# Kernel tuning notes

Measured on AMD Instinct MI355X. Metric: run time of the kernel, lower is better.

Reference implementation:

```python
import jax, jax.numpy as jnp
import numpy as np

B, S, D = 2, 2048, 1024
E, K = 8, 2
CAP_FACTOR = 1.25
HID = 4 * D


def _capacity(num_tokens: int) -> int:
    import math
    cap = math.floor(K * CAP_FACTOR * num_tokens / E)
    cap += cap % 2
    return max(int(cap), 2)


def setup_inputs() -> dict:
    key = jax.random.key(0)
    k1, k2, k3, k4 = jax.random.split(key, 4)
    x = jax.random.normal(k1, (B, S, D), dtype=jnp.float32)
    w_gate = jax.random.normal(k2, (D, E), dtype=jnp.float32) * 0.02
    w_fc = jax.random.normal(k3, (E, D, HID), dtype=jnp.float32) * 0.02
    w_proj = jax.random.normal(k4, (E, HID, D), dtype=jnp.float32) * 0.02
    return {"x": x, "w_gate": w_gate, "w_fc": w_fc, "w_proj": w_proj}


def _moe_forward(x, w_gate, w_fc, w_proj):
    b, s, d = x.shape
    T = b * s
    cap = _capacity(T)
    xf = x.astype(jnp.float32).reshape(T, d)

    # --- Router (fp32, eval mode: no noise) ---
    logits = xf @ w_gate                                   # [T, E]
    top_v, top_i = jax.lax.top_k(logits, K)                # [T, K]
    NEG = jnp.float32(-1e30)
    masked = jnp.full_like(logits, NEG)
    masked = masked.at[jnp.arange(T)[:, None], top_i].set(top_v)
    probs = jax.nn.softmax(masked, axis=-1)                # [T, E], zero off top-k

    # --- Capacity assignment: cumsum over (k-major, token) flattened order ---
    oh = jax.nn.one_hot(top_i, E, dtype=jnp.int32)         # [T, K, E]
    oh = jnp.transpose(oh, (1, 0, 2))                      # [K, T, E]
    rank = jnp.cumsum(oh.reshape(K * T, E), axis=0).reshape(K, T, E) - 1
    within = (oh > 0) & (rank < cap)                       # [K, T, E]
    rank_sel = jnp.sum(jnp.where(within, rank, 0), axis=-1)  # [K, T]
    kept = jnp.any(within, axis=-1)                        # [K, T]

    p = jnp.take_along_axis(probs, top_i, axis=-1).T       # [K, T]
    w = jnp.where(kept, p, 0.0)                            # combine weights

    e_idx = top_i.T                                        # [K, T]
    t_idx = jnp.broadcast_to(jnp.arange(T)[None, :], (K, T))

    # expert_weights[t, e, c] (sparse scatter == torch one-hot combine)
    expert_weights = jnp.zeros((T, E, cap), jnp.float32)
    expert_weights = expert_weights.at[t_idx.ravel(), e_idx.ravel(), rank_sel.ravel()].add(w.ravel())

    # dispatch: expert_batches[e, c, :] = x of token routed to (e, c)
    disp = jnp.where(kept, 1.0, 0.0).ravel()[:, None]      # [K*T, 1]
    expert_batches = jnp.zeros((E, cap, d), jnp.float32)
    expert_batches = expert_batches.at[e_idx.ravel(), rank_sel.ravel()].add(disp * xf[t_idx.ravel()])

    # --- Expert MLPs (batched GEMMs, exact GELU, no bias, eval dropout) ---
    h = jnp.einsum('ecd,edh->ech', expert_batches, w_fc)
    h = jax.nn.gelu(h, approximate=False)
    expert_out = jnp.einsum('ech,ehd->ecd', h, w_proj)      # [E, cap, d]

    # --- Combine: gather expert outputs back to tokens weighted by router prob ---
    gathered = expert_out[e_idx.ravel(), rank_sel.ravel()].reshape(K, T, d)
    out_flat = jnp.sum(w[:, :, None] * gathered, axis=0)    # [T, d]
    output = out_flat.reshape(b, s, d)

    # --- Load balance loss (Switch) ---
    probs_full = jax.nn.softmax(logits, axis=-1)
    prob_per_expert = jnp.mean(probs_full, axis=0)          # [E]
    tokens_per_expert = jax.lax.stop_gradient(
        jnp.sum((expert_weights > 0).astype(jnp.float32), axis=(0, 2)) / (T * K)
    )
    lb_loss = E * jnp.sum(prob_per_expert * tokens_per_expert)

    # --- Router z-loss ---
    z_loss = jnp.mean(jax.nn.logsumexp(logits, axis=-1) ** 2)
    return output, lb_loss, z_loss


def reference(x, w_gate, w_fc, w_proj):
    return _moe_forward(x, w_gate, w_fc, w_proj)
```

## Files before the change

kernel.cpp:

```cpp
#include <hip/hip_runtime.h>
#include <hip/hip_bf16.h>
#include <cstdint>
#include <cstddef>

#define T_TOK 4096
#define D_DIM 1024
#define E_EXP 8
#define KSEL 2
#define CAP 1280
#define HID_DIM 4096

typedef __attribute__((ext_vector_type(8))) __bf16 bf16x8;
typedef __attribute__((ext_vector_type(4))) float floatx4;

__device__ __forceinline__ unsigned short f2bf(float f) {
  unsigned int u = __builtin_bit_cast(unsigned int, f);
  u = (u + 0x7FFFu + ((u >> 16) & 1u)) >> 16;
  return (unsigned short)u;
}
__device__ __forceinline__ float bf2f(unsigned short h) {
  unsigned int u = ((unsigned int)h) << 16;
  return __builtin_bit_cast(float, u);
}

__global__ void router_kernel(const float* __restrict__ x, const float* __restrict__ wg,
                              int* __restrict__ top1, int* __restrict__ top2,
                              float* __restrict__ p0, float* __restrict__ p1,
                              float* __restrict__ probsum, float* __restrict__ zsum) {
  __shared__ float lps[E_EXP];
  __shared__ float lz;
  if (threadIdx.x < E_EXP) lps[threadIdx.x] = 0.f;
  if (threadIdx.x == 0) lz = 0.f;
  __syncthreads();
  int wave = threadIdx.x >> 6;
  int lane = threadIdx.x & 63;
  int t = blockIdx.x * 4 + wave;
  const float* xr = x + (size_t)t * D_DIM;
  float acc[E_EXP];
#pragma unroll
  for (int e = 0; e < E_EXP; ++e) acc[e] = 0.f;
  for (int j = 0; j < D_DIM / 64; ++j) {
    int i = lane + 64 * j;
    float xv = xr[i];
    const float4* wr = (const float4*)(wg + (size_t)i * E_EXP);
    float4 w0 = wr[0], w1 = wr[1];
    acc[0] += xv * w0.x; acc[1] += xv * w0.y; acc[2] += xv * w0.z; acc[3] += xv * w0.w;
    acc[4] += xv * w1.x; acc[5] += xv * w1.y; acc[6] += xv * w1.z; acc[7] += xv * w1.w;
  }
#pragma unroll
  for (int e = 0; e < E_EXP; ++e) {
#pragma unroll
    for (int s = 32; s > 0; s >>= 1) acc[e] += __shfl_xor(acc[e], s);
  }
  if (lane == 0) {
    int i1 = 0; float v1 = acc[0];
    for (int e = 1; e < E_EXP; ++e) if (acc[e] > v1) { v1 = acc[e]; i1 = e; }
    int i2 = -1; float v2 = -1e30f;
    for (int e = 0; e < E_EXP; ++e) if (e != i1 && acc[e] > v2) { v2 = acc[e]; i2 = e; }
    top1[t] = i1; top2[t] = i2;
    float dexp = expf(v2 - v1);
    p0[t] = 1.f / (1.f + dexp);
    p1[t] = dexp / (1.f + dexp);
    float pe[E_EXP]; float ssum = 0.f;
    for (int e = 0; e < E_EXP; ++e) { pe[e] = expf(acc[e] - v1); ssum += pe[e]; }
    float lse = logf(ssum) + v1;
    atomicAdd(&lz, lse * lse);
    float inv = 1.f / ssum;
    for (int e = 0; e < E_EXP; ++e) atomicAdd(&lps[e], pe[e] * inv);
  }
  __syncthreads();
  if (threadIdx.x < E_EXP) atomicAdd(&probsum[threadIdx.x], lps[threadIdx.x]);
  if (threadIdx.x == 0) atomicAdd(zsum, lz);
}

__global__ void scan_kernel(const int* __restrict__ top1, const int* __restrict__ top2,
                            int* __restrict__ rank0, int* __restrict__ rank1,
                            int* __restrict__ slot_token, int* __restrict__ cntk) {
  __shared__ int sc[256][E_EXP];
  int c = threadIdx.x;
  int e0l[16], e1l[16];
  int c0[E_EXP], c1[E_EXP];
#pragma unroll
  for (int e = 0; e < E_EXP; ++e) { c0[e] = 0; c1[e] = 0; }
#pragma unroll
  for (int j = 0; j < 16; ++j) {
    int t = c * 16 + j;
    int a = top1[t]; int b = top2[t];
    e0l[j] = a; e1l[j] = b;
    c0[a]++; c1[b]++;
  }
  for (int e = 0; e < E_EXP; ++e) sc[c][e] = c0[e];
  __syncthreads();
  for (int s = 1; s < 256; s <<= 1) {
    int tmp[E_EXP];
    if (c >= s) { for (int e = 0; e < E_EXP; ++e) tmp[e] = sc[c - s][e]; }
    __syncthreads();
    if (c >= s) { for (int e = 0; e < E_EXP; ++e) sc[c][e] += tmp[e]; }
    __syncthreads();
  }
  int off0[E_EXP], tot0[E_EXP];
  for (int e = 0; e < E_EXP; ++e) {
    off0[e] = (c > 0) ? sc[c - 1][e] : 0;
    tot0[e] = sc[255][e];
  }
  __syncthreads();
  for (int e = 0; e < E_EXP; ++e) sc[c][e] = c1[e];
  __syncthreads();
  for (int s = 1; s < 256; s <<= 1) {
    int tmp[E_EXP];
    if (c >= s) { for (int e = 0; e < E_EXP; ++e) tmp[e] = sc[c - s][e]; }
    __syncthreads();
    if (c >= s) { for (int e = 0; e < E_EXP; ++e) sc[c][e] += tmp[e]; }
    __syncthreads();
  }
  int off1[E_EXP], tot1[E_EXP];
  for (int e = 0; e < E_EXP; ++e) {
    off1[e] = (c > 0) ? sc[c - 1][e] : 0;
    tot1[e] = sc[255][e];
  }
  int run[E_EXP];
  for (int e = 0; e < E_EXP; ++e) run[e] = off0[e];
#pragma unroll
  for (int j = 0; j < 16; ++j) {
    int t = c * 16 + j;
    int e = e0l[j];
    int r = run[e]++;
    if (r < CAP) { rank0[t] = r; slot_token[e * CAP + r] = t; } else rank0[t] = -1;
  }
  for (int e = 0; e < E_EXP; ++e) run[e] = tot0[e] + off1[e];
#pragma unroll
  for (int j = 0; j < 16; ++j) {
    int t = c * 16 + j;
    int e = e1l[j];
    int r = run[e]++;
    if (r < CAP) { rank1[t] = r; slot_token[e * CAP + r] = t; } else rank1[t] = -1;
  }
  if (c == 0) {
    for (int e = 0; e < E_EXP; ++e) {
      int tot = tot0[e] + tot1[e];
      cntk[e] = tot < CAP ? tot : CAP;
    }
  }
}

__global__ void dispatch_kernel(const float* __restrict__ x, const int* __restrict__ slot_token,
                                unsigned short* __restrict__ batch) {
  int slot = blockIdx.x;
  int t = slot_token[slot];
  int d = threadIdx.x * 4;
  ushort4 o;
  if (t >= 0) {
    float4 v = *(const float4*)(x + (size_t)t * D_DIM + d);
    o.x = f2bf(v.x); o.y = f2bf(v.y); o.z = f2bf(v.z); o.w = f2bf(v.w);
  } else {
    o.x = 0; o.y = 0; o.z = 0; o.w = 0;
  }
  *(ushort4*)(batch + (size_t)slot * D_DIM + d) = o;
}

__global__ void transpose_convert(const float* __restrict__ in, unsigned short* __restrict__ out,
                                  int R, int C) {
  __shared__ float tile[32][33];
  int b = blockIdx.z;
  int c0 = blockIdx.x * 32;
  int r0 = blockIdx.y * 32;
  int tx = threadIdx.x;
  int ty = threadIdx.y;
  const float* ip = in + (size_t)b * R * C;
  unsigned short* op = out + (size_t)b * R * C;
#pragma unroll
  for (int j = 0; j < 4; ++j)
    tile[ty + 8 * j][tx] = ip[(size_t)(r0 + ty + 8 * j) * C + (c0 + tx)];
  __syncthreads();
#pragma unroll
  for (int j = 0; j < 4; ++j)
    op[(size_t)(c0 + ty + 8 * j) * R + (r0 + tx)] = f2bf(tile[tx][ty + 8 * j]);
}

template <int KD, int NN, bool GELU>
__global__ __launch_bounds__(256) void gemm_bt(const unsigned short* __restrict__ A,
                                               const unsigned short* __restrict__ BT,
                                               unsigned short* __restrict__ Cd,
                                               const int* __restrict__ cntk) {
  int e = blockIdx.z;
  int m0 = blockIdx.x * 128;
  int n0 = blockIdx.y * 128;
  if (m0 >= cntk[e]) return;
  const unsigned short* Ae = A + (size_t)e * CAP * KD;
  const unsigned short* Be = BT + (size_t)e * NN * KD;
  unsigned short* Ce = Cd + (size_t)e * CAP * NN;
  __shared__ unsigned short As[128 * 40];
  __shared__ unsigned short Bs[128 * 40];
  int tid = threadIdx.x;
  int lane = tid & 63;
  int wv = tid >> 6;
  int wm = (wv & 1) * 64;
  int wn = (wv >> 1) * 64;
  int mrow = lane & 15;
  int kq = (lane >> 4) * 8;
  floatx4 acc[4][4];
#pragma unroll
  for (int i = 0; i < 4; ++i)
#pragma unroll
    for (int j = 0; j < 4; ++j) {
      floatx4 z = {0.f, 0.f, 0.f, 0.f};
      acc[i][j] = z;
    }
  for (int k0 = 0; k0 < KD; k0 += 32) {
#pragma unroll
    for (int i = 0; i < 2; ++i) {
      int ch = i * 256 + tid;
      int r = ch >> 2;
      int cc = (ch & 3) * 8;
      *(bf16x8*)(&As[r * 40 + cc]) = *(const bf16x8*)(&Ae[(size_t)(m0 + r) * KD + k0 + cc]);
      *(bf16x8*)(&Bs[r * 40 + cc]) = *(const bf16x8*)(&Be[(size_t)(n0 + r) * KD + k0 + cc]);
    }
    __syncthreads();
    bf16x8 af[4], bfr[4];
#pragma unroll
    for (int mt = 0; mt < 4; ++mt)
      af[mt] = *(const bf16x8*)(&As[(wm + mt * 16 + mrow) * 40 + kq]);
#pragma unroll
    for (int nt = 0; nt < 4; ++nt)
      bfr[nt] = *(const bf16x8*)(&Bs[(wn + nt * 16 + mrow) * 40 + kq]);
#pragma unroll
    for (int mt = 0; mt < 4; ++mt)
#pragma unroll
      for (int nt = 0; nt < 4; ++nt)
        acc[mt][nt] = __builtin_amdgcn_mfma_f32_16x16x32_bf16(af[mt], bfr[nt], acc[mt][nt], 0, 0, 0);
    __syncthreads();
  }
  int crow = (lane >> 4) * 4;
  int ccol = lane & 15;
#pragma unroll
  for (int mt = 0; mt < 4; ++mt)
#pragma unroll
    for (int nt = 0; nt < 4; ++nt)
#pragma unroll
      for (int r = 0; r < 4; ++r) {
        float v = acc[mt][nt][r];
        if (GELU) v = 0.5f * v * (1.f + erff(v * 0.70710678118654752f));
        Ce[(size_t)(m0 + wm + mt * 16 + crow + r) * NN + (n0 + wn + nt * 16 + ccol)] = f2bf(v);
      }
}

__global__ void combine_kernel(const unsigned short* __restrict__ EO,
                               const int* __restrict__ top1, const int* __restrict__ top2,
                               const float* __restrict__ p0, const float* __restrict__ p1,
                               const int* __restrict__ rank0, const int* __restrict__ rank1,
                               float* __restrict__ out) {
  int t = blockIdx.x;
  int d = threadIdx.x * 4;
  float a0 = 0.f, a1 = 0.f, a2 = 0.f, a3 = 0.f;
  int r0 = rank0[t];
  if (r0 >= 0) {
    float w = p0[t];
    ushort4 v = *(const ushort4*)(EO + ((size_t)top1[t] * CAP + r0) * D_DIM + d);
    a0 += w * bf2f(v.x); a1 += w * bf2f(v.y); a2 += w * bf2f(v.z); a3 += w * bf2f(v.w);
  }
  int r1 = rank1[t];
  if (r1 >= 0) {
    float w = p1[t];
    ushort4 v = *(const ushort4*)(EO + ((size_t)top2[t] * CAP + r1) * D_DIM + d);
    a0 += w * bf2f(v.x); a1 += w * bf2f(v.y); a2 += w * bf2f(v.z); a3 += w * bf2f(v.w);
  }
  float4 o; o.x = a0; o.y = a1; o.z = a2; o.w = a3;
  *(float4*)(out + (size_t)t * D_DIM + d) = o;
}

__global__ void finalize_kernel(const float* __restrict__ probsum, const float* __restrict__ zsum,
                                const int* __restrict__ cntk, float* __restrict__ out) {
  if (threadIdx.x == 0) {
    float lb = 0.f;
    for (int e = 0; e < E_EXP; ++e)
      lb += (probsum[e] / (float)T_TOK) * ((float)cntk[e] / (float)(T_TOK * KSEL));
    out[(size_t)T_TOK * D_DIM] = lb * (float)E_EXP;
    out[(size_t)T_TOK * D_DIM + 1] = zsum[0] / (float)T_TOK;
  }
}

extern "C" void kernel_launch(void* const* d_in, const int* in_sizes, int n_in,
                              void* d_out, int out_size, void* d_ws, size_t ws_size,
                              hipStream_t stream) {
  const float* x = (const float*)d_in[0];
  const float* w_gate = (const float*)d_in[1];
  const float* w_fc = (const float*)d_in[2];
  const float* w_proj = (const float*)d_in[3];
  float* out = (float*)d_out;
  char* ws = (char*)d_ws;

  float* probsum = (float*)(ws + 0);
  float* zsum    = (float*)(ws + 32);
  int*   cntk    = (int*)(ws + 64);
  int*   top1    = (int*)(ws + 4096);
  int*   top2    = (int*)(ws + 20480);
  float* p0      = (float*)(ws + 36864);
  float* p1      = (float*)(ws + 53248);
  int*   rank0   = (int*)(ws + 69632);
  int*   rank1   = (int*)(ws + 86016);
  int*   slot    = (int*)(ws + 102400);
  unsigned short* batch = (unsigned short*)(ws + 262144);
  unsigned short* H     = (unsigned short*)(ws + 262144 + 20971520);
  unsigned short* EO    = (unsigned short*)(ws + 262144 + 20971520 + 83886080);
  unsigned short* W     = (unsigned short*)(ws + 262144 + 20971520 + 83886080 + 20971520);

  hipMemsetAsync(ws, 0, 4096, stream);
  hipMemsetAsync(slot, 0xFF, E_EXP * CAP * sizeof(int), stream);

  router_kernel<<<T_TOK / 4, 256, 0, stream>>>(x, w_gate, top1, top2, p0, p1, probsum, zsum);
  scan_kernel<<<1, 256, 0, stream>>>(top1, top2, rank0, rank1, slot, cntk);
  dispatch_kernel<<<E_EXP * CAP, 256, 0, stream>>>(x, slot, batch);

  transpose_convert<<<dim3(HID_DIM / 32, D_DIM / 32, E_EXP), dim3(32, 8), 0, stream>>>(w_fc, W, D_DIM, HID_DIM);
  gemm_bt<D_DIM, HID_DIM, true><<<dim3(CAP / 128, HID_DIM / 128, E_EXP), 256, 0, stream>>>(batch, W, H, cntk);

  transpose_convert<<<dim3(D_DIM / 32, HID_DIM / 32, E_EXP), dim3(32, 8), 0, stream>>>(w_proj, W, HID_DIM, D_DIM);
  gemm_bt<HID_DIM, D_DIM, false><<<dim3(CAP / 128, D_DIM / 128, E_EXP), 256, 0, stream>>>(H, W, EO, cntk);

  combine_kernel<<<T_TOK, 256, 0, stream>>>(EO, top1, top2, p0, p1, rank0, rank1, out);
  finalize_kernel<<<1, 64, 0, stream>>>(probsum, zsum, cntk, out);
}
```

Before: 666.0 us.

## Use direct global-to-LDS loads with XOR swizzle and grouped tile order in expert GEMMs

The expert GEMM now stages A and B tiles with global_load_lds (bypassing registers), using an XOR-swizzled unpadded LDS layout to avoid bank conflicts. Blocks are flattened into a 1D grid with experts interleaved and N-tiles grouped, which is meant to improve cache reuse. The weight transpose kernel is also widened to 64x64 tiles with vectorized float4 loads and 16-byte stores. Correctness now depends on the swizzle matching between the load and the read, and on the async LDS writes being complete at the barrier with no explicit vmcnt wait.

```diff
diff --git a/kernel.cpp b/kernel.cpp
--- a/kernel.cpp
+++ b/kernel.cpp
@@ -11,6 +11,7 @@
 #define HID_DIM 4096
 
 typedef __attribute__((ext_vector_type(8))) __bf16 bf16x8;
+typedef __attribute__((ext_vector_type(8))) unsigned short ushort8;
 typedef __attribute__((ext_vector_type(4))) float floatx4;
 
 __device__ __forceinline__ unsigned short f2bf(float f) {
@@ -21,6 +22,12 @@
 __device__ __forceinline__ float bf2f(unsigned short h) {
   unsigned int u = ((unsigned int)h) << 16;
   return __builtin_bit_cast(float, u);
+}
+
+__device__ __forceinline__ void async16(const unsigned short* g, unsigned short* l) {
+  __builtin_amdgcn_global_load_lds(
+      (const __attribute__((address_space(1))) unsigned int*)g,
+      (__attribute__((address_space(3))) unsigned int*)l, 16, 0, 0);
 }
 
 __global__ void router_kernel(const float* __restrict__ x, const float* __restrict__ wg,
@@ -158,46 +165,66 @@
   *(ushort4*)(batch + (size_t)slot * D_DIM + d) = o;
 }
 
-__global__ void transpose_convert(const float* __restrict__ in, unsigned short* __restrict__ out,
-                                  int R, int C) {
-  __shared__ float tile[32][33];
+__global__ __launch_bounds__(256) void transpose_convert(const float* __restrict__ in,
+                                                         unsigned short* __restrict__ out,
+                                                         int R, int C) {
+  __shared__ float tile[64][65];
   int b = blockIdx.z;
-  int c0 = blockIdx.x * 32;
-  int r0 = blockIdx.y * 32;
-  int tx = threadIdx.x;
-  int ty = threadIdx.y;
+  int c0 = blockIdx.x * 64;
+  int r0 = blockIdx.y * 64;
   const float* ip = in + (size_t)b * R * C;
   unsigned short* op = out + (size_t)b * R * C;
-#pragma unroll
-  for (int j = 0; j < 4; ++j)
-    tile[ty + 8 * j][tx] = ip[(size_t)(r0 + ty + 8 * j) * C + (c0 + tx)];
-  __syncthreads();
-#pragma unroll
-  for (int j = 0; j < 4; ++j)
-    op[(size_t)(c0 + ty + 8 * j) * R + (r0 + tx)] = f2bf(tile[tx][ty + 8 * j]);
-}
-
-template <int KD, int NN, bool GELU>
-__global__ __launch_bounds__(256) void gemm_bt(const unsigned short* __restrict__ A,
-                                               const unsigned short* __restrict__ BT,
-                                               unsigned short* __restrict__ Cd,
-                                               const int* __restrict__ cntk) {
-  int e = blockIdx.z;
-  int m0 = blockIdx.x * 128;
-  int n0 = blockIdx.y * 128;
+  int tid = threadIdx.x;
+  int rr = tid >> 4;
+  int cc = (tid & 15) * 4;
+#pragma unroll
+  for (int it = 0; it < 4; ++it) {
+    int r = rr + it * 16;
+    float4 v = *(const float4*)(ip + (size_t)(r0 + r) * C + c0 + cc);
+    tile[r][cc] = v.x; tile[r][cc + 1] = v.y; tile[r][cc + 2] = v.z; tile[r][cc + 3] = v.w;
+  }
+  __syncthreads();
+  int c = tid >> 2;
+  int rq = (tid & 3) * 16;
+  unsigned short vals[16];
+#pragma unroll
+  for (int j = 0; j < 16; ++j) vals[j] = f2bf(tile[rq + j][c]);
+  unsigned short* dst = op + (size_t)(c0 + c) * R + r0 + rq;
+  *(ushort8*)dst = *(ushort8*)&vals[0];
+  *(ushort8*)(dst + 8) = *(ushort8*)&vals[8];
+}
+
+template <int KD, int NN, int NG_TILES, bool GELU>
+__global__ __launch_bounds__(256) void gemm_alds(const unsigned short* __restrict__ A,
+                                                 const unsigned short* __restrict__ BT,
+                                                 unsigned short* __restrict__ Cd,
+                                                 const int* __restrict__ cntk) {
+  constexpr int MT = CAP / 128;
+  constexpr int GRP = MT * NG_TILES;
+  int bid = blockIdx.x;
+  int e = bid & 7;
+  int slot = bid >> 3;
+  int ng = slot / GRP;
+  int rem = slot - ng * GRP;
+  int mm = rem / NG_TILES;
+  int nw = rem - mm * NG_TILES;
+  int m0 = mm * 128;
+  int n0 = (ng * NG_TILES + nw) * 128;
   if (m0 >= cntk[e]) return;
   const unsigned short* Ae = A + (size_t)e * CAP * KD;
   const unsigned short* Be = BT + (size_t)e * NN * KD;
   unsigned short* Ce = Cd + (size_t)e * CAP * NN;
-  __shared__ unsigned short As[128 * 40];
-  __shared__ unsigned short Bs[128 * 40];
+  __shared__ unsigned short As[128 * 32];
+  __shared__ unsigned short Bs[128 * 32];
   int tid = threadIdx.x;
   int lane = tid & 63;
   int wv = tid >> 6;
   int wm = (wv & 1) * 64;
   int wn = (wv >> 1) * 64;
   int mrow = lane & 15;
-  int kq = (lane >> 4) * 8;
+  int kqb = lane >> 4;
+  int sx = (mrow >> 1) & 3;
+  int kb = (kqb ^ sx) * 8;
   floatx4 acc[4][4];
 #pragma unroll
   for (int i = 0; i < 4; ++i)
@@ -209,20 +236,21 @@
   for (int k0 = 0; k0 < KD; k0 += 32) {
 #pragma unroll
     for (int i = 0; i < 2; ++i) {
-      int ch = i * 256 + tid;
+      int chw = i * 256 + wv * 64;
+      int ch = chw + lane;
       int r = ch >> 2;
-      int cc = (ch & 3) * 8;
-      *(bf16x8*)(&As[r * 40 + cc]) = *(const bf16x8*)(&Ae[(size_t)(m0 + r) * KD + k0 + cc]);
-      *(bf16x8*)(&Bs[r * 40 + cc]) = *(const bf16x8*)(&Be[(size_t)(n0 + r) * KD + k0 + cc]);
+      int cbs = (ch & 3) ^ ((r >> 1) & 3);
+      async16(&Ae[(size_t)(m0 + r) * KD + k0 + cbs * 8], &As[chw * 8]);
+      async16(&Be[(size_t)(n0 + r) * KD + k0 + cbs * 8], &Bs[chw * 8]);
     }
     __syncthreads();
     bf16x8 af[4], bfr[4];
 #pragma unroll
     for (int mt = 0; mt < 4; ++mt)
-      af[mt] = *(const bf16x8*)(&As[(wm + mt * 16 + mrow) * 40 + kq]);
+      af[mt] = *(const bf16x8*)(&As[(wm + mt * 16 + mrow) * 32 + kb]);
 #pragma unroll
     for (int nt = 0; nt < 4; ++nt)
-      bfr[nt] = *(const bf16x8*)(&Bs[(wn + nt * 16 + mrow) * 40 + kq]);
+      bfr[nt] = *(const bf16x8*)(&Bs[(wn + nt * 16 + mrow) * 32 + kb]);
 #pragma unroll
     for (int mt = 0; mt < 4; ++mt)
 #pragma unroll
@@ -311,11 +339,11 @@
   scan_kernel<<<1, 256, 0, stream>>>(top1, top2, rank0, rank1, slot, cntk);
   dispatch_kernel<<<E_EXP * CAP, 256, 0, stream>>>(x, slot, batch);
 
-  transpose_convert<<<dim3(HID_DIM / 32, D_DIM / 32, E_EXP), dim3(32, 8), 0, stream>>>(w_fc, W, D_DIM, HID_DIM);
-  gemm_bt<D_DIM, HID_DIM, true><<<dim3(CAP / 128, HID_DIM / 128, E_EXP), 256, 0, stream>>>(batch, W, H, cntk);
-
-  transpose_convert<<<dim3(D_DIM / 32, HID_DIM / 32, E_EXP), dim3(32, 8), 0, stream>>>(w_proj, W, HID_DIM, D_DIM);
-  gemm_bt<HID_DIM, D_DIM, false><<<dim3(CAP / 128, D_DIM / 128, E_EXP), 256, 0, stream>>>(H, W, EO, cntk);
+  transpose_convert<<<dim3(HID_DIM / 64, D_DIM / 64, E_EXP), 256, 0, stream>>>(w_fc, W, D_DIM, HID_DIM);
+  gemm_alds<D_DIM, HID_DIM, 4, true><<<8 * (HID_DIM / 128 / 4) * (CAP / 128) * 4, 256, 0, stream>>>(batch, W, H, cntk);
+
+  transpose_convert<<<dim3(D_DIM / 64, HID_DIM / 64, E_EXP), 256, 0, stream>>>(w_proj, W, HID_DIM, D_DIM);
+  gemm_alds<HID_DIM, D_DIM, 2, false><<<8 * (D_DIM / 128 / 2) * (CAP / 128) * 2, 256, 0, stream>>>(H, W, EO, cntk);
 
   combine_kernel<<<T_TOK, 256, 0, stream>>>(EO, top1, top2, p0, p1, rank0, rank1, out);
   finalize_kernel<<<1, 64, 0, stream>>>(probsum, zsum, cntk, out);
```

Measured after the change: 584.1 us. 1.14x faster.
